# Performance work log

Measured on AMD Instinct MI355X. Metric: run time of the kernel, lower is better.

The kernel has to match this reference:

```python
import jax, jax.numpy as jnp
import numpy as np

N_NODES = 100000
N_EDGES = 1600000
D = 128


def setup_inputs() -> dict:
    key = jax.random.key(0)
    ks = jax.random.split(key, 6)
    x = jax.random.normal(ks[0], (N_NODES, D), dtype=jnp.float32)
    edge_index = jax.random.randint(ks[1], (2, N_EDGES), 0, N_NODES, dtype=jnp.int32)
    # nn.Linear weights: [out, in], bias [out]
    W1 = jax.random.normal(ks[2], (D, D), dtype=jnp.float32) * (1.0 / np.sqrt(D))
    b1 = jax.random.normal(ks[3], (D,), dtype=jnp.float32) * 0.01
    W2 = jax.random.normal(ks[4], (D, D), dtype=jnp.float32) * (1.0 / np.sqrt(D))
    b2 = jax.random.normal(ks[5], (D,), dtype=jnp.float32) * 0.01
    return {"x": x, "edge_index": edge_index, "W1": W1, "b1": b1, "W2": W2, "b2": b2}


def _gin_conv(x, src, dst, W, b, num_nodes):
    # sum aggregation of source features into destination nodes
    agg = jax.ops.segment_sum(x[src], dst, num_segments=num_nodes)  # [N, d]
    # eps = 0 (PyG GINConv default): (1+eps)*x_i + sum_j x_j, then Linear
    return (x + agg) @ W.T + b


def reference(x, edge_index, W1, b1, W2, b2):
    src, dst = edge_index[0], edge_index[1]
    n = x.shape[0]
    hid = _gin_conv(x, src, dst, W1, b1, n)
    out = _gin_conv(hid, src, dst, W2, b2, n)
    return (out, hid)
```

## Files before the change

kernel.cpp:

```cpp
#include <hip/hip_runtime.h>


#define DFEAT 128
#define BSHIFT 8
#define NB_MAX 512
#define CAP 8192
#define LROWS 136
#define AGG_BLOCKS 2048

typedef __attribute__((ext_vector_type(8))) short short8;
typedef __attribute__((ext_vector_type(4))) float f32x4;

__device__ __forceinline__ float bf2f(unsigned short u) {
    union { unsigned int i; float f; } c;
    c.i = ((unsigned int)u) << 16;
    return c.f;
}
__device__ __forceinline__ unsigned short f2b(float f) {
    union { float f; unsigned int i; } c;
    c.f = f;
    unsigned int u = c.i;
    u = (u + 0x7FFFu + ((u >> 16) & 1u)) >> 16;
    return (unsigned short)u;
}


__global__ __launch_bounds__(256) void scatter_cast(const int* __restrict__ src,
                                                    const int* __restrict__ dst,
                                                    int* __restrict__ bcur,
                                                    int* __restrict__ ebuf, int E,
                                                    int nscat,
                                                    const float* __restrict__ x,
                                                    unsigned short* __restrict__ xb,
                                                    int total4, int nzero) {
    int tid = threadIdx.x;
    if (blockIdx.x >= nscat) {
        int i = (blockIdx.x - nscat) * 256 + tid;
        if (i < total4) {
            float4 v = ((const float4*)x)[i];
            ushort4 o;
            o.x = f2b(v.x); o.y = f2b(v.y); o.z = f2b(v.z); o.w = f2b(v.w);
            ((ushort4*)xb)[i] = o;
        }
        if (blockIdx.x == nscat && tid < 32)
            ((ushort4*)xb)[(size_t)nzero * 32 + tid] = make_ushort4(0, 0, 0, 0);
        return;
    }
    __shared__ int lh[NB_MAX];
    for (int i = tid; i < NB_MAX; i += 256) lh[i] = 0;
    __syncthreads();
    int e0 = blockIdx.x * 4096;
    int e1 = min(e0 + 4096, E);
    int s[16], d[16];
    #pragma unroll
    for (int j = 0; j < 16; j++) {
        int e = e0 + tid + 256 * j;
        if (e < e1) { s[j] = src[e]; d[j] = dst[e]; atomicAdd(&lh[d[j] >> BSHIFT], 1); }
    }
    __syncthreads();
    for (int i = tid; i < NB_MAX; i += 256) {
        int c = lh[i];
        lh[i] = c ? (i * CAP + atomicAdd(&bcur[i], c)) : 0;
    }
    __syncthreads();
    #pragma unroll
    for (int j = 0; j < 16; j++) {
        int e = e0 + tid + 256 * j;
        if (e < e1) {
            int b = d[j] >> BSHIFT;
            int p = atomicAdd(&lh[b], 1);
            if (p < (b + 1) * CAP) ebuf[p] = (s[j] << 8) | (d[j] & 255);
        }
    }
}


__global__ __launch_bounds__(256) void csr_prep(const int* __restrict__ ebuf,
                                                const int* __restrict__ bcur,
                                                int2* __restrict__ rpse,
                                                int* __restrict__ esrc, int n, int nbk,
                                                const float* __restrict__ W1,
                                                const float* __restrict__ W2,
                                                const float* __restrict__ b1,
                                                unsigned short* __restrict__ Wb1,
                                                unsigned short* __restrict__ Wcb,
                                                float* __restrict__ w2b1) {
    int tid = threadIdx.x;
    if (blockIdx.x >= nbk) {
        __shared__ float red[256];
        int bb = blockIdx.x - nbk;
        int i = bb * 2 + (tid >> 7);
        int j = tid & 127;
        float s = 0.f;
        #pragma unroll 4
        for (int k = 0; k < 128; k++) s += W2[i * 128 + k] * W1[k * 128 + j];
        Wcb[i * 128 + j] = f2b(s);
        Wb1[i * 128 + j] = f2b(W1[i * 128 + j]);
        red[tid] = W2[i * 128 + j] * b1[j];
        __syncthreads();
        if (j == 0) {
            float t = 0.f;
            for (int k = 0; k < 128; k++) t += red[tid + k];
            w2b1[i] = t;
        }
        return;
    }
    __shared__ int hist[256];
    __shared__ int wsum[4];
    __shared__ int woff2[4];
    int b = blockIdx.x;
    int nbase = b << BSHIFT;
    int e0 = b * CAP;
    int e1 = e0 + min(bcur[b], CAP);
    hist[tid] = 0;
    __syncthreads();
    for (int e = e0 + tid; e < e1; e += 256)
        atomicAdd(&hist[ebuf[e] & 255], 1);
    __syncthreads();
    int v = hist[tid];
    int lane = tid & 63, wid = tid >> 6;
    int inc = v;
    #pragma unroll
    for (int off = 1; off < 64; off <<= 1) {
        int u = __shfl_up(inc, off, 64);
        if (lane >= off) inc += u;
    }
    if (lane == 63) wsum[wid] = inc;
    __syncthreads();
    if (tid == 0) {
        int run = 0;
        #pragma unroll
        for (int w = 0; w < 4; w++) { woff2[w] = run; run += wsum[w]; }
    }
    __syncthreads();
    int excl = woff2[wid] + inc - v;
    int node = nbase + tid;
    if (node < n) rpse[node] = make_int2(e0 + excl, e0 + excl + v);
    __syncthreads();
    hist[tid] = excl;
    __syncthreads();
    for (int e = e0 + tid; e < e1; e += 256) {
        int le = ebuf[e];
        int p = atomicAdd(&hist[le & 255], 1);
        esrc[e0 + p] = ((unsigned int)le) >> 8;
    }
}


__global__ __launch_bounds__(256) void fused_agg_gemm1(
        const ushort4* __restrict__ zin4, const int2* __restrict__ rpse,
        const int* __restrict__ esrc, const unsigned short* __restrict__ Wb,
        const float* __restrict__ bias, unsigned short* __restrict__ zout,
        float* __restrict__ out, int n, int ntiles) {
    __shared__ __align__(16) short lt[16 * LROWS];
    int w = threadIdx.x >> 6;
    int wl = threadIdx.x & 63;
    int gl = wl & 15, q = wl >> 4;
    int gbase = wl & 48;
    unsigned lb = (unsigned)gl * 16u;
    int lrow = w * 4 + q;
    const char* zb = (const char*)zin4;
    const int stride = gridDim.x;

    if (blockIdx.x == 0 && threadIdx.x < 16) {
        short8 z8;
        #pragma unroll
        for (int t = 0; t < 8; t++) z8[t] = 0;
        *(short8*)((char*)zout + (unsigned)n * 256u + threadIdx.x * 16) = z8;
    }

    float bb[2];
    #pragma unroll
    for (int cc = 0; cc < 2; cc++) bb[cc] = bias[(w * 2 + cc) * 16 + gl];

    int t = blockIdx.x;
    int node = t * 16 + lrow;
    int2 se = make_int2(0, 0);
    if (t < ntiles && node < n) se = rpse[node];
    int deg0 = se.y - se.x;
    int ei0 = (t < ntiles && node < n && gl < deg0) ? esrc[se.x + gl] : n;
    int ei1 = (t < ntiles && node < n && gl + 16 < deg0) ? esrc[se.x + gl + 16] : n;

    for (; t < ntiles; ) {
        int tn = t + stride;
        int node_n = tn * 16 + lrow;
        int2 se_n = make_int2(0, 0);
        if (tn < ntiles && node_n < n) se_n = rpse[node_n];

        int node_c = node < n ? node : n;
        float a[8];
        short8 sv = *(const short8*)(zb + (unsigned)node_c * 256u + lb);
        #pragma unroll
        for (int tt = 0; tt < 8; tt++) a[tt] = bf2f((unsigned short)sv[tt]);

        unsigned off[16];
        short8 vv[16];
        #pragma unroll
        for (int k = 0; k < 16; k++)
            off[k] = (unsigned)__shfl(ei0, gbase + k) * 256u + lb;
        #pragma unroll
        for (int k = 0; k < 16; k++) vv[k] = *(const short8*)(zb + off[k]);

        int deg_n = se_n.y - se_n.x;
        int ei0_n = n, ei1_n = n;
        if (tn < ntiles && node_n < n) {
            if (gl < deg_n)      ei0_n = esrc[se_n.x + gl];
            if (gl + 16 < deg_n) ei1_n = esrc[se_n.x + gl + 16];
        }

        #pragma unroll
        for (int k = 0; k < 16; k++) {
            #pragma unroll
            for (int tt = 0; tt < 8; tt++) a[tt] += bf2f((unsigned short)vv[k][tt]);
        }
        int deg = se.y - se.x;
        if (deg > 16) {
            unsigned o2[16];
            short8 v2[16];
            #pragma unroll
            for (int k = 0; k < 16; k++)
                o2[k] = (unsigned)__shfl(ei1, gbase + k) * 256u + lb;
            #pragma unroll
            for (int k = 0; k < 16; k++) v2[k] = *(const short8*)(zb + o2[k]);
            #pragma unroll
            for (int k = 0; k < 16; k++) {
                #pragma unroll
                for (int tt = 0; tt < 8; tt++) a[tt] += bf2f((unsigned short)v2[k][tt]);
            }
        }
        for (int rb = 32; rb < deg; rb += 16) {
            int eidx = (rb + gl < deg) ? esrc[se.x + rb + gl] : n;
            unsigned o2[16];
            short8 v2[16];
            #pragma unroll
            for (int k = 0; k < 16; k++)
                o2[k] = (unsigned)__shfl(eidx, gbase + k) * 256u + lb;
            #pragma unroll
            for (int k = 0; k < 16; k++) v2[k] = *(const short8*)(zb + o2[k]);
            #pragma unroll
            for (int k = 0; k < 16; k++) {
                #pragma unroll
                for (int tt = 0; tt < 8; tt++) a[tt] += bf2f((unsigned short)v2[k][tt]);
            }
        }

        short8 o;
        #pragma unroll
        for (int tt = 0; tt < 8; tt++) o[tt] = (short)f2b(a[tt]);
        *(short8*)((char*)lt + lrow * (LROWS * 2) + lb) = o;
        if (node < n) *(short8*)((char*)zout + (unsigned)node * 256u + lb) = o;
        __syncthreads();

        int m = gl;
        const short* ap = lt + m * LROWS + q * 8;
        short8 a0 = *(const short8*)(ap);
        short8 a1 = *(const short8*)(ap + 32);
        short8 a2 = *(const short8*)(ap + 64);
        short8 a3 = *(const short8*)(ap + 96);
        f32x4 acc[2];
        #pragma unroll
        for (int cc = 0; cc < 2; cc++) acc[cc] = (f32x4){0.f, 0.f, 0.f, 0.f};
        #pragma unroll
        for (int cc = 0; cc < 2; cc++) {
            int c = w * 2 + cc;
            const short* wp = (const short*)Wb + (c * 16 + m) * 128 + q * 8;
            short8 b0 = *(const short8*)(wp);
            short8 b1v = *(const short8*)(wp + 32);
            short8 b2v = *(const short8*)(wp + 64);
            short8 b3v = *(const short8*)(wp + 96);
            acc[cc] = __builtin_amdgcn_mfma_f32_16x16x32_bf16(a0, b0, acc[cc], 0, 0, 0);
            acc[cc] = __builtin_amdgcn_mfma_f32_16x16x32_bf16(a1, b1v, acc[cc], 0, 0, 0);
            acc[cc] = __builtin_amdgcn_mfma_f32_16x16x32_bf16(a2, b2v, acc[cc], 0, 0, 0);
            acc[cc] = __builtin_amdgcn_mfma_f32_16x16x32_bf16(a3, b3v, acc[cc], 0, 0, 0);
        }
        int row0 = t * 16 + q * 4;
        #pragma unroll
        for (int cc = 0; cc < 2; cc++) {
            int col = (w * 2 + cc) * 16 + m;
            #pragma unroll
            for (int r = 0; r < 4; r++) {
                int nd = row0 + r;
                if (nd < n) out[(size_t)nd * 128 + col] = acc[cc][r] + bb[cc];
            }
        }
        __syncthreads();

        se = se_n; ei0 = ei0_n; ei1 = ei1_n; node = node_n; t = tn;
    }
}

__global__ __launch_bounds__(256) void fused_agg_gemm2(
        const ushort4* __restrict__ zin4, const int2* __restrict__ rpse,
        const int* __restrict__ esrc, const unsigned short* __restrict__ Wb,
        const float* __restrict__ w2b1, const float* __restrict__ bias2,
        float* __restrict__ out, int n, int ntiles) {
    __shared__ __align__(16) short lt[16 * LROWS];
    int w = threadIdx.x >> 6;
    int wl = threadIdx.x & 63;
    int gl = wl & 15, q = wl >> 4;
    int gbase = wl & 48;
    unsigned lb = (unsigned)gl * 16u;
    int lrow = w * 4 + q;
    const char* zb = (const char*)zin4;
    const int stride = gridDim.x;

    float wb2[2], bb2[2];
    #pragma unroll
    for (int cc = 0; cc < 2; cc++) {
        int col = (w * 2 + cc) * 16 + gl;
        wb2[cc] = w2b1[col];
        bb2[cc] = bias2[col];
    }

    int t = blockIdx.x;
    int node = t * 16 + lrow;
    int2 se = make_int2(0, 0);
    if (t < ntiles && node < n) se = rpse[node];
    int deg0 = se.y - se.x;
    int ei0 = (t < ntiles && node < n && gl < deg0) ? esrc[se.x + gl] : n;
    int ei1 = (t < ntiles && node < n && gl + 16 < deg0) ? esrc[se.x + gl + 16] : n;

    for (; t < ntiles; ) {
        int tn = t + stride;
        int node_n = tn * 16 + lrow;
        int2 se_n = make_int2(0, 0);
        if (tn < ntiles && node_n < n) se_n = rpse[node_n];

        int node_c = node < n ? node : n;
        float a[8];
        short8 sv = *(const short8*)(zb + (unsigned)node_c * 256u + lb);
        #pragma unroll
        for (int tt = 0; tt < 8; tt++) a[tt] = bf2f((unsigned short)sv[tt]);

        unsigned off[16];
        short8 vv[16];
        #pragma unroll
        for (int k = 0; k < 16; k++)
            off[k] = (unsigned)__shfl(ei0, gbase + k) * 256u + lb;
        #pragma unroll
        for (int k = 0; k < 16; k++) vv[k] = *(const short8*)(zb + off[k]);

        int deg_n = se_n.y - se_n.x;
        int ei0_n = n, ei1_n = n;
        if (tn < ntiles && node_n < n) {
            if (gl < deg_n)      ei0_n = esrc[se_n.x + gl];
            if (gl + 16 < deg_n) ei1_n = esrc[se_n.x + gl + 16];
        }

        #pragma unroll
        for (int k = 0; k < 16; k++) {
            #pragma unroll
            for (int tt = 0; tt < 8; tt++) a[tt] += bf2f((unsigned short)vv[k][tt]);
        }
        int deg = se.y - se.x;
        if (deg > 16) {
            unsigned o2[16];
            short8 v2[16];
            #pragma unroll
            for (int k = 0; k < 16; k++)
                o2[k] = (unsigned)__shfl(ei1, gbase + k) * 256u + lb;
            #pragma unroll
            for (int k = 0; k < 16; k++) v2[k] = *(const short8*)(zb + o2[k]);
            #pragma unroll
            for (int k = 0; k < 16; k++) {
                #pragma unroll
                for (int tt = 0; tt < 8; tt++) a[tt] += bf2f((unsigned short)v2[k][tt]);
            }
        }
        for (int rb = 32; rb < deg; rb += 16) {
            int eidx = (rb + gl < deg) ? esrc[se.x + rb + gl] : n;
            unsigned o2[16];
            short8 v2[16];
            #pragma unroll
            for (int k = 0; k < 16; k++)
                o2[k] = (unsigned)__shfl(eidx, gbase + k) * 256u + lb;
            #pragma unroll
            for (int k = 0; k < 16; k++) v2[k] = *(const short8*)(zb + o2[k]);
            #pragma unroll
            for (int k = 0; k < 16; k++) {
                #pragma unroll
                for (int tt = 0; tt < 8; tt++) a[tt] += bf2f((unsigned short)v2[k][tt]);
            }
        }

        short8 o;
        #pragma unroll
        for (int tt = 0; tt < 8; tt++) o[tt] = (short)f2b(a[tt]);
        *(short8*)((char*)lt + lrow * (LROWS * 2) + lb) = o;
        __syncthreads();

        int m = gl;
        const short* ap = lt + m * LROWS + q * 8;
        short8 a0 = *(const short8*)(ap);
        short8 a1 = *(const short8*)(ap + 32);
        short8 a2 = *(const short8*)(ap + 64);
        short8 a3 = *(const short8*)(ap + 96);
        f32x4 acc[2];
        #pragma unroll
        for (int cc = 0; cc < 2; cc++) acc[cc] = (f32x4){0.f, 0.f, 0.f, 0.f};
        #pragma unroll
        for (int cc = 0; cc < 2; cc++) {
            int c = w * 2 + cc;
            const short* wp = (const short*)Wb + (c * 16 + m) * 128 + q * 8;
            short8 b0 = *(const short8*)(wp);
            short8 b1v = *(const short8*)(wp + 32);
            short8 b2v = *(const short8*)(wp + 64);
            short8 b3v = *(const short8*)(wp + 96);
            acc[cc] = __builtin_amdgcn_mfma_f32_16x16x32_bf16(a0, b0, acc[cc], 0, 0, 0);
            acc[cc] = __builtin_amdgcn_mfma_f32_16x16x32_bf16(a1, b1v, acc[cc], 0, 0, 0);
            acc[cc] = __builtin_amdgcn_mfma_f32_16x16x32_bf16(a2, b2v, acc[cc], 0, 0, 0);
            acc[cc] = __builtin_amdgcn_mfma_f32_16x16x32_bf16(a3, b3v, acc[cc], 0, 0, 0);
        }
        int row0 = t * 16 + q * 4;
        float degf[4];
        #pragma unroll
        for (int r = 0; r < 4; r++) {
            int nd = row0 + r;
            if (nd < n) {
                int2 s2 = rpse[nd];
                degf[r] = (float)(1 + s2.y - s2.x);
            } else degf[r] = 0.f;
        }
        #pragma unroll
        for (int cc = 0; cc < 2; cc++) {
            int col = (w * 2 + cc) * 16 + m;
            #pragma unroll
            for (int r = 0; r < 4; r++) {
                int nd = row0 + r;
                if (nd < n) out[(size_t)nd * 128 + col] = acc[cc][r] + degf[r] * wb2[cc] + bb2[cc];
            }
        }
        __syncthreads();

        se = se_n; ei0 = ei0_n; ei1 = ei1_n; node = node_n; t = tn;
    }
}


extern "C" void kernel_launch(void* const* d_in, const int* in_sizes, int n_in,
                              void* d_out, int out_size, void* d_ws, size_t ws_size,
                              hipStream_t stream) {
    const float* x  = (const float*)d_in[0];
    const int*   ei = (const int*)d_in[1];
    const float* W1 = (const float*)d_in[2];
    const float* b1 = (const float*)d_in[3];
    const float* W2 = (const float*)d_in[4];
    const float* b2 = (const float*)d_in[5];

    const int n = in_sizes[0] / DFEAT;
    const int E = in_sizes[1] / 2;
    const int* src = ei;
    const int* dst = ei + E;
    const int nbuckets = (n + (1 << BSHIFT) - 1) >> BSHIFT;

    float* out = (float*)d_out;
    float* hid = out + (size_t)n * DFEAT;

    unsigned short* xb = (unsigned short*)out;

    char* w = (char*)d_ws;
    const size_t szB = (size_t)n * DFEAT * sizeof(unsigned short);
    const size_t szB1 = szB + 4096;
    unsigned short* z1b = (unsigned short*)w;
    int* ebuf = (int*)(w + szB1);
    int* esrc = (int*)(w + szB1 + szB);
    int2* rpse = (int2*)(esrc + (size_t)nbuckets * CAP);
    int* bcur = (int*)(rpse + n);
    char* wp = (char*)(bcur + NB_MAX);
    unsigned short* Wb1 = (unsigned short*)wp;
    unsigned short* Wcb = Wb1 + DFEAT * DFEAT;
    float* w2b1 = (float*)(Wcb + DFEAT * DFEAT);

    const int cast_blocks = (n * 32 + 255) / 256;
    hipMemsetAsync(bcur, 0, nbuckets * sizeof(int), stream);
    scatter_cast<<<nbuckets + cast_blocks, 256, 0, stream>>>(
        src, dst, bcur, ebuf, E, nbuckets, x, xb, n * 32, n);
    csr_prep<<<nbuckets + 64, 256, 0, stream>>>(
        ebuf, bcur, rpse, esrc, n, nbuckets, W1, W2, b1, Wb1, Wcb, w2b1);

    const int ntiles = (n + 15) / 16;
    const int fb = AGG_BLOCKS;
    fused_agg_gemm1<<<fb, 256, 0, stream>>>(
        (const ushort4*)xb, rpse, esrc, Wb1, b1, z1b, hid, n, ntiles);
    fused_agg_gemm2<<<fb, 256, 0, stream>>>(
        (const ushort4*)z1b, rpse, esrc, Wcb, w2b1, b2, out, n, ntiles);
}
```

Baseline: 326.2 us.

## Fuse CSR bucket sort into first aggregation+GEMM kernel with 64-node buckets

Destination buckets shrink from 256 to 64 nodes. The per-bucket counting sort now runs inside the first aggregation/GEMM kernel, which keeps the sorted source list in shared memory and still writes rpse and esrc for the second layer. The weight preprocessing moves into the scatter/cast kernel, so one launch and a round trip of esrc through global memory are removed. The cost is a larger shared-memory footprint per block and no cross-tile prefetch of edge indices. Per-bucket capacity also drops to 2048 edges, which leaves less headroom for skewed degree distributions.

```diff
diff --git a/kernel.cpp b/kernel.cpp
--- a/kernel.cpp
+++ b/kernel.cpp
@@ -2,9 +2,10 @@
 
 
 #define DFEAT 128
-#define BSHIFT 8
-#define NB_MAX 512
-#define CAP 8192
+#define BSHIFT 6
+#define BNODES 64
+#define NB_MAX 2048
+#define CAP 2048
 #define LROWS 136
 #define AGG_BLOCKS 2048
 
@@ -25,70 +26,30 @@
 }
 
 
-__global__ __launch_bounds__(256) void scatter_cast(const int* __restrict__ src,
-                                                    const int* __restrict__ dst,
-                                                    int* __restrict__ bcur,
-                                                    int* __restrict__ ebuf, int E,
-                                                    int nscat,
-                                                    const float* __restrict__ x,
-                                                    unsigned short* __restrict__ xb,
-                                                    int total4, int nzero) {
+__global__ __launch_bounds__(256) void scatter_cast_prep(
+        const int* __restrict__ src, const int* __restrict__ dst,
+        int* __restrict__ bcur, int* __restrict__ ebuf, int E, int nscat, int nbk,
+        const float* __restrict__ x, unsigned short* __restrict__ xb,
+        int total4, int nzero,
+        const float* __restrict__ W1, const float* __restrict__ W2,
+        const float* __restrict__ b1, unsigned short* __restrict__ Wb1,
+        unsigned short* __restrict__ Wcb, float* __restrict__ w2b1) {
     int tid = threadIdx.x;
-    if (blockIdx.x >= nscat) {
-        int i = (blockIdx.x - nscat) * 256 + tid;
+    if (blockIdx.x >= nscat + 64) {
+        int i = (blockIdx.x - nscat - 64) * 256 + tid;
         if (i < total4) {
             float4 v = ((const float4*)x)[i];
             ushort4 o;
             o.x = f2b(v.x); o.y = f2b(v.y); o.z = f2b(v.z); o.w = f2b(v.w);
             ((ushort4*)xb)[i] = o;
         }
-        if (blockIdx.x == nscat && tid < 32)
+        if (blockIdx.x == nscat + 64 && tid < 32)
             ((ushort4*)xb)[(size_t)nzero * 32 + tid] = make_ushort4(0, 0, 0, 0);
         return;
     }
-    __shared__ int lh[NB_MAX];
-    for (int i = tid; i < NB_MAX; i += 256) lh[i] = 0;
-    __syncthreads();
-    int e0 = blockIdx.x * 4096;
-    int e1 = min(e0 + 4096, E);
-    int s[16], d[16];
-    #pragma unroll
-    for (int j = 0; j < 16; j++) {
-        int e = e0 + tid + 256 * j;
-        if (e < e1) { s[j] = src[e]; d[j] = dst[e]; atomicAdd(&lh[d[j] >> BSHIFT], 1); }
-    }
-    __syncthreads();
-    for (int i = tid; i < NB_MAX; i += 256) {
-        int c = lh[i];
-        lh[i] = c ? (i * CAP + atomicAdd(&bcur[i], c)) : 0;
-    }
-    __syncthreads();
-    #pragma unroll
-    for (int j = 0; j < 16; j++) {
-        int e = e0 + tid + 256 * j;
-        if (e < e1) {
-            int b = d[j] >> BSHIFT;
-            int p = atomicAdd(&lh[b], 1);
-            if (p < (b + 1) * CAP) ebuf[p] = (s[j] << 8) | (d[j] & 255);
-        }
-    }
-}
-
-
-__global__ __launch_bounds__(256) void csr_prep(const int* __restrict__ ebuf,
-                                                const int* __restrict__ bcur,
-                                                int2* __restrict__ rpse,
-                                                int* __restrict__ esrc, int n, int nbk,
-                                                const float* __restrict__ W1,
-                                                const float* __restrict__ W2,
-                                                const float* __restrict__ b1,
-                                                unsigned short* __restrict__ Wb1,
-                                                unsigned short* __restrict__ Wcb,
-                                                float* __restrict__ w2b1) {
-    int tid = threadIdx.x;
-    if (blockIdx.x >= nbk) {
+    if (blockIdx.x >= nscat) {
         __shared__ float red[256];
-        int bb = blockIdx.x - nbk;
+        int bb = blockIdx.x - nscat;
         int i = bb * 2 + (tid >> 7);
         int j = tid & 127;
         float s = 0.f;
@@ -105,154 +66,172 @@
         }
         return;
     }
-    __shared__ int hist[256];
-    __shared__ int wsum[4];
-    __shared__ int woff2[4];
+    __shared__ int lh[NB_MAX];
+    for (int i = tid; i < nbk; i += 256) lh[i] = 0;
+    __syncthreads();
+    int e0 = blockIdx.x * 4096;
+    int e1 = min(e0 + 4096, E);
+    int s[16], d[16];
+    #pragma unroll
+    for (int j = 0; j < 16; j++) {
+        int e = e0 + tid + 256 * j;
+        if (e < e1) { s[j] = src[e]; d[j] = dst[e]; atomicAdd(&lh[d[j] >> BSHIFT], 1); }
+    }
+    __syncthreads();
+    for (int i = tid; i < nbk; i += 256) {
+        int c = lh[i];
+        lh[i] = c ? (i * CAP + atomicAdd(&bcur[i], c)) : 0;
+    }
+    __syncthreads();
+    #pragma unroll
+    for (int j = 0; j < 16; j++) {
+        int e = e0 + tid + 256 * j;
+        if (e < e1) {
+            int b = d[j] >> BSHIFT;
+            int p = atomicAdd(&lh[b], 1);
+            if (p < (b + 1) * CAP) ebuf[p] = (s[j] << 6) | (d[j] & 63);
+        }
+    }
+}
+
+
+__global__ __launch_bounds__(256) void fused_csr_agg_gemm1(
+        const int* __restrict__ ebuf, const int* __restrict__ bcur,
+        const ushort4* __restrict__ zin4, const unsigned short* __restrict__ Wb,
+        const float* __restrict__ bias, int2* __restrict__ rpse,
+        int* __restrict__ esrc, unsigned short* __restrict__ zout,
+        float* __restrict__ out, int n) {
+    __shared__ int esrc_s[CAP];
+    __shared__ __align__(16) short lt[64 * LROWS];
+    __shared__ int cursor[64];
+    __shared__ int exl_s[64];
+    __shared__ int deg_s[64];
+    int tid = threadIdx.x;
     int b = blockIdx.x;
-    int nbase = b << BSHIFT;
-    int e0 = b * CAP;
-    int e1 = e0 + min(bcur[b], CAP);
-    hist[tid] = 0;
-    __syncthreads();
-    for (int e = e0 + tid; e < e1; e += 256)
-        atomicAdd(&hist[ebuf[e] & 255], 1);
-    __syncthreads();
-    int v = hist[tid];
-    int lane = tid & 63, wid = tid >> 6;
-    int inc = v;
-    #pragma unroll
-    for (int off = 1; off < 64; off <<= 1) {
-        int u = __shfl_up(inc, off, 64);
-        if (lane >= off) inc += u;
-    }
-    if (lane == 63) wsum[wid] = inc;
-    __syncthreads();
-    if (tid == 0) {
-        int run = 0;
-        #pragma unroll
-        for (int w = 0; w < 4; w++) { woff2[w] = run; run += wsum[w]; }
-    }
-    __syncthreads();
-    int excl = woff2[wid] + inc - v;
-    int node = nbase + tid;
-    if (node < n) rpse[node] = make_int2(e0 + excl, e0 + excl + v);
-    __syncthreads();
-    hist[tid] = excl;
-    __syncthreads();
-    for (int e = e0 + tid; e < e1; e += 256) {
-        int le = ebuf[e];
-        int p = atomicAdd(&hist[le & 255], 1);
-        esrc[e0 + p] = ((unsigned int)le) >> 8;
-    }
-}
-
-
-__global__ __launch_bounds__(256) void fused_agg_gemm1(
-        const ushort4* __restrict__ zin4, const int2* __restrict__ rpse,
-        const int* __restrict__ esrc, const unsigned short* __restrict__ Wb,
-        const float* __restrict__ bias, unsigned short* __restrict__ zout,
-        float* __restrict__ out, int n, int ntiles) {
-    __shared__ __align__(16) short lt[16 * LROWS];
-    int w = threadIdx.x >> 6;
-    int wl = threadIdx.x & 63;
+    int e0b = b * CAP;
+    int cnt = min(bcur[b], CAP);
+
+    if (b == 0 && tid < 16) {
+        short8 z8;
+        #pragma unroll
+        for (int t = 0; t < 8; t++) z8[t] = 0;
+        *(short8*)((char*)zout + (unsigned)n * 256u + tid * 16) = z8;
+    }
+
+    if (tid < 64) cursor[tid] = 0;
+    __syncthreads();
+    for (int e = tid; e < cnt; e += 256)
+        atomicAdd(&cursor[ebuf[e0b + e] & 63], 1);
+    __syncthreads();
+    if (tid < 64) {
+        int v = cursor[tid];
+        int inc = v;
+        #pragma unroll
+        for (int off = 1; off < 64; off <<= 1) {
+            int u = __shfl_up(inc, off, 64);
+            if (tid >= off) inc += u;
+        }
+        int excl = inc - v;
+        exl_s[tid] = excl;
+        deg_s[tid] = v;
+        int node = b * 64 + tid;
+        if (node < n) rpse[node] = make_int2(e0b + excl, e0b + excl + v);
+    }
+    __syncthreads();
+    if (tid < 64) cursor[tid] = exl_s[tid];
+    __syncthreads();
+    for (int e = tid; e < cnt; e += 256) {
+        int le = ebuf[e0b + e];
+        int p = atomicAdd(&cursor[le & 63], 1);
+        int sv = ((unsigned)le) >> 6;
+        esrc_s[p] = sv;
+        esrc[e0b + p] = sv;
+    }
+    __syncthreads();
+
+    int w = tid >> 6, wl = tid & 63;
     int gl = wl & 15, q = wl >> 4;
     int gbase = wl & 48;
     unsigned lb = (unsigned)gl * 16u;
-    int lrow = w * 4 + q;
     const char* zb = (const char*)zin4;
-    const int stride = gridDim.x;
-
-    if (blockIdx.x == 0 && threadIdx.x < 16) {
-        short8 z8;
-        #pragma unroll
-        for (int t = 0; t < 8; t++) z8[t] = 0;
-        *(short8*)((char*)zout + (unsigned)n * 256u + threadIdx.x * 16) = z8;
-    }
-
+    for (int it = 0; it < 4; ++it) {
+        int li = w * 16 + it * 4 + q;
+        int node = b * 64 + li;
+        int deg = deg_s[li], eb = exl_s[li];
+        int node_c = node < n ? node : n;
+        float a[8];
+        short8 svr = *(const short8*)(zb + (unsigned)node_c * 256u + lb);
+        #pragma unroll
+        for (int tt = 0; tt < 8; tt++) a[tt] = bf2f((unsigned short)svr[tt]);
+        int ei0 = (gl < deg) ? esrc_s[eb + gl] : n;
+        int ei1 = (gl + 16 < deg) ? esrc_s[eb + gl + 16] : n;
+        {
+            unsigned off[16];
+            short8 vv[16];
+            #pragma unroll
+            for (int k = 0; k < 16; k++)
+                off[k] = (unsigned)__shfl(ei0, gbase + k) * 256u + lb;
+            #pragma unroll
+            for (int k = 0; k < 16; k++) vv[k] = *(const short8*)(zb + off[k]);
+            #pragma unroll
+            for (int k = 0; k < 16; k++) {
+                #pragma unroll
+                for (int tt = 0; tt < 8; tt++) a[tt] += bf2f((unsigned short)vv[k][tt]);
+            }
+        }
+        if (deg > 16) {
+            unsigned off[16];
+            short8 vv[16];
+            #pragma unroll
+            for (int k = 0; k < 16; k++)
+                off[k] = (unsigned)__shfl(ei1, gbase + k) * 256u + lb;
+            #pragma unroll
+            for (int k = 0; k < 16; k++) vv[k] = *(const short8*)(zb + off[k]);
+            #pragma unroll
+            for (int k = 0; k < 16; k++) {
+                #pragma unroll
+                for (int tt = 0; tt < 8; tt++) a[tt] += bf2f((unsigned short)vv[k][tt]);
+            }
+        }
+        for (int rb = 32; rb < deg; rb += 16) {
+            int eidx = (rb + gl < deg) ? esrc_s[eb + rb + gl] : n;
+            unsigned off[16];
+            short8 vv[16];
+            #pragma unroll
+            for (int k = 0; k < 16; k++)
+                off[k] = (unsigned)__shfl(eidx, gbase + k) * 256u + lb;
+            #pragma unroll
+            for (int k = 0; k < 16; k++) vv[k] = *(const short8*)(zb + off[k]);
+            #pragma unroll
+            for (int k = 0; k < 16; k++) {
+                #pragma unroll
+                for (int tt = 0; tt < 8; tt++) a[tt] += bf2f((unsigned short)vv[k][tt]);
+            }
+        }
+        short8 o;
+        #pragma unroll
+        for (int tt = 0; tt < 8; tt++) o[tt] = (short)f2b(a[tt]);
+        *(short8*)((char*)lt + li * (LROWS * 2) + lb) = o;
+        if (node < n) *(short8*)((char*)zout + (unsigned)node * 256u + lb) = o;
+    }
+    __syncthreads();
+
+    int m = gl;
+    short8 B[2][4];
     float bb[2];
     #pragma unroll
-    for (int cc = 0; cc < 2; cc++) bb[cc] = bias[(w * 2 + cc) * 16 + gl];
-
-    int t = blockIdx.x;
-    int node = t * 16 + lrow;
-    int2 se = make_int2(0, 0);
-    if (t < ntiles && node < n) se = rpse[node];
-    int deg0 = se.y - se.x;
-    int ei0 = (t < ntiles && node < n && gl < deg0) ? esrc[se.x + gl] : n;
-    int ei1 = (t < ntiles && node < n && gl + 16 < deg0) ? esrc[se.x + gl + 16] : n;
-
-    for (; t < ntiles; ) {
-        int tn = t + stride;
-        int node_n = tn * 16 + lrow;
-        int2 se_n = make_int2(0, 0);
-        if (tn < ntiles && node_n < n) se_n = rpse[node_n];
-
-        int node_c = node < n ? node : n;
-        float a[8];
-        short8 sv = *(const short8*)(zb + (unsigned)node_c * 256u + lb);
-        #pragma unroll
-        for (int tt = 0; tt < 8; tt++) a[tt] = bf2f((unsigned short)sv[tt]);
-
-        unsigned off[16];
-        short8 vv[16];
-        #pragma unroll
-        for (int k = 0; k < 16; k++)
-            off[k] = (unsigned)__shfl(ei0, gbase + k) * 256u + lb;
-        #pragma unroll
-        for (int k = 0; k < 16; k++) vv[k] = *(const short8*)(zb + off[k]);
-
-        int deg_n = se_n.y - se_n.x;
-        int ei0_n = n, ei1_n = n;
-        if (tn < ntiles && node_n < n) {
-            if (gl < deg_n)      ei0_n = esrc[se_n.x + gl];
-            if (gl + 16 < deg_n) ei1_n = esrc[se_n.x + gl + 16];
-        }
-
-        #pragma unroll
-        for (int k = 0; k < 16; k++) {
-            #pragma unroll
-            for (int tt = 0; tt < 8; tt++) a[tt] += bf2f((unsigned short)vv[k][tt]);
-        }
-        int deg = se.y - se.x;
-        if (deg > 16) {
-            unsigned o2[16];
-            short8 v2[16];
-            #pragma unroll
-            for (int k = 0; k < 16; k++)
-                o2[k] = (unsigned)__shfl(ei1, gbase + k) * 256u + lb;
-            #pragma unroll
-            for (int k = 0; k < 16; k++) v2[k] = *(const short8*)(zb + o2[k]);
-            #pragma unroll
-            for (int k = 0; k < 16; k++) {
-                #pragma unroll
-                for (int tt = 0; tt < 8; tt++) a[tt] += bf2f((unsigned short)v2[k][tt]);
-            }
-        }
-        for (int rb = 32; rb < deg; rb += 16) {
-            int eidx = (rb + gl < deg) ? esrc[se.x + rb + gl] : n;
-            unsigned o2[16];
-            short8 v2[16];
-            #pragma unroll
-            for (int k = 0; k < 16; k++)
-                o2[k] = (unsigned)__shfl(eidx, gbase + k) * 256u + lb;
-            #pragma unroll
-            for (int k = 0; k < 16; k++) v2[k] = *(const short8*)(zb + o2[k]);
-            #pragma unroll
-            for (int k = 0; k < 16; k++) {
-                #pragma unroll
-                for (int tt = 0; tt < 8; tt++) a[tt] += bf2f((unsigned short)v2[k][tt]);
-            }
-        }
-
-        short8 o;
-        #pragma unroll
-        for (int tt = 0; tt < 8; tt++) o[tt] = (short)f2b(a[tt]);
-        *(short8*)((char*)lt + lrow * (LROWS * 2) + lb) = o;
-        if (node < n) *(short8*)((char*)zout + (unsigned)node * 256u + lb) = o;
-        __syncthreads();
-
-        int m = gl;
-        const short* ap = lt + m * LROWS + q * 8;
+    for (int cc = 0; cc < 2; cc++) {
+        int c = w * 2 + cc;
+        const short* wp = (const short*)Wb + (c * 16 + m) * 128 + q * 8;
+        B[cc][0] = *(const short8*)(wp);
+        B[cc][1] = *(const short8*)(wp + 32);
+        B[cc][2] = *(const short8*)(wp + 64);
+        B[cc][3] = *(const short8*)(wp + 96);
+        bb[cc] = bias[c * 16 + m];
+    }
+    #pragma unroll
+    for (int st = 0; st < 4; ++st) {
+        const short* ap = lt + (st * 16 + m) * LROWS + q * 8;
         short8 a0 = *(const short8*)(ap);
         short8 a1 = *(const short8*)(ap + 32);
         short8 a2 = *(const short8*)(ap + 64);
@@ -262,18 +241,12 @@
         for (int cc = 0; cc < 2; cc++) acc[cc] = (f32x4){0.f, 0.f, 0.f, 0.f};
         #pragma unroll
         for (int cc = 0; cc < 2; cc++) {
-            int c = w * 2 + cc;
-            const short* wp = (const short*)Wb + (c * 16 + m) * 128 + q * 8;
-            short8 b0 = *(const short8*)(wp);
-            short8 b1v = *(const short8*)(wp + 32);
-            short8 b2v = *(const short8*)(wp + 64);
-            short8 b3v = *(const short8*)(wp + 96);
-            acc[cc] = __builtin_amdgcn_mfma_f32_16x16x32_bf16(a0, b0, acc[cc], 0, 0, 0);
-            acc[cc] = __builtin_amdgcn_mfma_f32_16x16x32_bf16(a1, b1v, acc[cc], 0, 0, 0);
-            acc[cc] = __builtin_amdgcn_mfma_f32_16x16x32_bf16(a2, b2v, acc[cc], 0, 0, 0);
-            acc[cc] = __builtin_amdgcn_mfma_f32_16x16x32_bf16(a3, b3v, acc[cc], 0, 0, 0);
-        }
-        int row0 = t * 16 + q * 4;
+            acc[cc] = __builtin_amdgcn_mfma_f32_16x16x32_bf16(a0, B[cc][0], acc[cc], 0, 0, 0);
+            acc[cc] = __builtin_amdgcn_mfma_f32_16x16x32_bf16(a1, B[cc][1], acc[cc], 0, 0, 0);
+            acc[cc] = __builtin_amdgcn_mfma_f32_16x16x32_bf16(a2, B[cc][2], acc[cc], 0, 0, 0);
+            acc[cc] = __builtin_amdgcn_mfma_f32_16x16x32_bf16(a3, B[cc][3], acc[cc], 0, 0, 0);
+        }
+        int row0 = b * 64 + st * 16 + q * 4;
         #pragma unroll
         for (int cc = 0; cc < 2; cc++) {
             int col = (w * 2 + cc) * 16 + m;
@@ -283,11 +256,9 @@
                 if (nd < n) out[(size_t)nd * 128 + col] = acc[cc][r] + bb[cc];
             }
         }
-        __syncthreads();
-
-        se = se_n; ei0 = ei0_n; ei1 = ei1_n; node = node_n; t = tn;
-    }
-}
+    }
+}
+
 
 __global__ __launch_bounds__(256) void fused_agg_gemm2(
         const ushort4* __restrict__ zin4, const int2* __restrict__ rpse,
@@ -451,7 +422,7 @@
     const int E = in_sizes[1] / 2;
     const int* src = ei;
     const int* dst = ei + E;
-    const int nbuckets = (n + (1 << BSHIFT) - 1) >> BSHIFT;
+    const int nbuckets = (n + BNODES - 1) / BNODES;
 
     float* out = (float*)d_out;
     float* hid = out + (size_t)n * DFEAT;
@@ -471,17 +442,17 @@
     unsigned short* Wcb = Wb1 + DFEAT * DFEAT;
     float* w2b1 = (float*)(Wcb + DFEAT * DFEAT);
 
+    const int nscat = (E + 4095) / 4096;
     const int cast_blocks = (n * 32 + 255) / 256;
     hipMemsetAsync(bcur, 0, nbuckets * sizeof(int), stream);
-    scatter_cast<<<nbuckets + cast_blocks, 256, 0, stream>>>(
-        src, dst, bcur, ebuf, E, nbuckets, x, xb, n * 32, n);
-    csr_prep<<<nbuckets + 64, 256, 0, stream>>>(
-        ebuf, bcur, rpse, esrc, n, nbuckets, W1, W2, b1, Wb1, Wcb, w2b1);
+    scatter_cast_prep<<<nscat + 64 + cast_blocks, 256, 0, stream>>>(
+        src, dst, bcur, ebuf, E, nscat, nbuckets, x, xb, n * 32, n,
+        W1, W2, b1, Wb1, Wcb, w2b1);
+
+    fused_csr_agg_gemm1<<<nbuckets, 256, 0, stream>>>(
+        ebuf, bcur, (const ushort4*)xb, Wb1, b1, rpse, esrc, z1b, hid, n);
 
     const int ntiles = (n + 15) / 16;
-    const int fb = AGG_BLOCKS;
-    fused_agg_gemm1<<<fb, 256, 0, stream>>>(
-        (const ushort4*)xb, rpse, esrc, Wb1, b1, z1b, hid, n, ntiles);
-    fused_agg_gemm2<<<fb, 256, 0, stream>>>(
+    fused_agg_gemm2<<<AGG_BLOCKS, 256, 0, stream>>>(
         (const ushort4*)z1b, rpse, esrc, Wcb, w2b1, b2, out, n, ntiles);
 }
```

Measured after the change: 328.3 us. Within noise of the previous version (+0.6%).

## Split CSR prep per bucket into four quarter-blocks for more parallelism

Applied to the files above, without the earlier changes.

The CSR build kernel now launches four blocks per destination bucket. Each block handles the 64 destination nodes of one quarter and writes into a fixed QCAP-sized sub-region of the bucket's edge range. This raises block count and parallelism in the histogram, scan and scatter phases. The cost is that each block rereads the whole bucket's edge buffer, so those reads happen four times. A quarter holding more than QCAP edges would spill into the next quarter's region. The scatter kernel's grid size is now derived from the edge count instead of the bucket count.

```diff
diff --git a/kernel.cpp b/kernel.cpp
--- a/kernel.cpp
+++ b/kernel.cpp
@@ -5,6 +5,7 @@
 #define BSHIFT 8
 #define NB_MAX 512
 #define CAP 8192
+#define QCAP 2048
 #define LROWS 136
 #define AGG_BLOCKS 2048
 
@@ -75,20 +76,20 @@
 }
 
 
-__global__ __launch_bounds__(256) void csr_prep(const int* __restrict__ ebuf,
-                                                const int* __restrict__ bcur,
-                                                int2* __restrict__ rpse,
-                                                int* __restrict__ esrc, int n, int nbk,
-                                                const float* __restrict__ W1,
-                                                const float* __restrict__ W2,
-                                                const float* __restrict__ b1,
-                                                unsigned short* __restrict__ Wb1,
-                                                unsigned short* __restrict__ Wcb,
-                                                float* __restrict__ w2b1) {
+__global__ __launch_bounds__(256) void csr_prep_q(const int* __restrict__ ebuf,
+                                                  const int* __restrict__ bcur,
+                                                  int2* __restrict__ rpse,
+                                                  int* __restrict__ esrc, int n, int nq,
+                                                  const float* __restrict__ W1,
+                                                  const float* __restrict__ W2,
+                                                  const float* __restrict__ b1,
+                                                  unsigned short* __restrict__ Wb1,
+                                                  unsigned short* __restrict__ Wcb,
+                                                  float* __restrict__ w2b1) {
     int tid = threadIdx.x;
-    if (blockIdx.x >= nbk) {
+    if (blockIdx.x >= nq) {
         __shared__ float red[256];
-        int bb = blockIdx.x - nbk;
+        int bb = blockIdx.x - nq;
         int i = bb * 2 + (tid >> 7);
         int j = tid & 127;
         float s = 0.f;
@@ -105,44 +106,42 @@
         }
         return;
     }
-    __shared__ int hist[256];
-    __shared__ int wsum[4];
-    __shared__ int woff2[4];
-    int b = blockIdx.x;
-    int nbase = b << BSHIFT;
-    int e0 = b * CAP;
-    int e1 = e0 + min(bcur[b], CAP);
-    hist[tid] = 0;
-    __syncthreads();
-    for (int e = e0 + tid; e < e1; e += 256)
-        atomicAdd(&hist[ebuf[e] & 255], 1);
-    __syncthreads();
-    int v = hist[tid];
-    int lane = tid & 63, wid = tid >> 6;
-    int inc = v;
-    #pragma unroll
-    for (int off = 1; off < 64; off <<= 1) {
-        int u = __shfl_up(inc, off, 64);
-        if (lane >= off) inc += u;
-    }
-    if (lane == 63) wsum[wid] = inc;
-    __syncthreads();
-    if (tid == 0) {
-        int run = 0;
-        #pragma unroll
-        for (int w = 0; w < 4; w++) { woff2[w] = run; run += wsum[w]; }
-    }
-    __syncthreads();
-    int excl = woff2[wid] + inc - v;
-    int node = nbase + tid;
-    if (node < n) rpse[node] = make_int2(e0 + excl, e0 + excl + v);
-    __syncthreads();
-    hist[tid] = excl;
-    __syncthreads();
-    for (int e = e0 + tid; e < e1; e += 256) {
-        int le = ebuf[e];
-        int p = atomicAdd(&hist[le & 255], 1);
-        esrc[e0 + p] = ((unsigned int)le) >> 8;
+    __shared__ int hist[64];
+    __shared__ int excl_s[64];
+    int b = blockIdx.x, cb = b >> 2, qq = b & 3;
+    int e0 = cb * CAP;
+    int cnt = min(bcur[cb], CAP);
+    int qbase = e0 + qq * QCAP;
+    if (tid < 64) hist[tid] = 0;
+    __syncthreads();
+    for (int e = tid; e < cnt; e += 256) {
+        int d = ebuf[e0 + e] & 255;
+        if ((d >> 6) == qq) atomicAdd(&hist[d & 63], 1);
+    }
+    __syncthreads();
+    if (tid < 64) {
+        int v = hist[tid];
+        int inc = v;
+        #pragma unroll
+        for (int off = 1; off < 64; off <<= 1) {
+            int u = __shfl_up(inc, off, 64);
+            if (tid >= off) inc += u;
+        }
+        int excl = inc - v;
+        excl_s[tid] = excl;
+        int node = cb * 256 + qq * 64 + tid;
+        if (node < n) rpse[node] = make_int2(qbase + excl, qbase + excl + v);
+    }
+    __syncthreads();
+    if (tid < 64) hist[tid] = excl_s[tid];
+    __syncthreads();
+    for (int e = tid; e < cnt; e += 256) {
+        int code = ebuf[e0 + e];
+        int d = code & 255;
+        if ((d >> 6) == qq) {
+            int p = atomicAdd(&hist[d & 63], 1);
+            esrc[qbase + p] = ((unsigned)code) >> 8;
+        }
     }
 }
 
@@ -451,7 +450,7 @@
     const int E = in_sizes[1] / 2;
     const int* src = ei;
     const int* dst = ei + E;
-    const int nbuckets = (n + (1 << BSHIFT) - 1) >> BSHIFT;
+    const int nbuckets = (n + 255) >> BSHIFT;
 
     float* out = (float*)d_out;
     float* hid = out + (size_t)n * DFEAT;
@@ -471,17 +470,19 @@
     unsigned short* Wcb = Wb1 + DFEAT * DFEAT;
     float* w2b1 = (float*)(Wcb + DFEAT * DFEAT);
 
+    const int nscat = (E + 4095) / 4096;
     const int cast_blocks = (n * 32 + 255) / 256;
     hipMemsetAsync(bcur, 0, nbuckets * sizeof(int), stream);
-    scatter_cast<<<nbuckets + cast_blocks, 256, 0, stream>>>(
-        src, dst, bcur, ebuf, E, nbuckets, x, xb, n * 32, n);
-    csr_prep<<<nbuckets + 64, 256, 0, stream>>>(
-        ebuf, bcur, rpse, esrc, n, nbuckets, W1, W2, b1, Wb1, Wcb, w2b1);
+    scatter_cast<<<nscat + cast_blocks, 256, 0, stream>>>(
+        src, dst, bcur, ebuf, E, nscat, x, xb, n * 32, n);
+
+    const int nq = nbuckets * 4;
+    csr_prep_q<<<nq + 64, 256, 0, stream>>>(
+        ebuf, bcur, rpse, esrc, n, nq, W1, W2, b1, Wb1, Wcb, w2b1);
 
     const int ntiles = (n + 15) / 16;
-    const int fb = AGG_BLOCKS;
-    fused_agg_gemm1<<<fb, 256, 0, stream>>>(
+    fused_agg_gemm1<<<AGG_BLOCKS, 256, 0, stream>>>(
         (const ushort4*)xb, rpse, esrc, Wb1, b1, z1b, hid, n, ntiles);
-    fused_agg_gemm2<<<fb, 256, 0, stream>>>(
+    fused_agg_gemm2<<<AGG_BLOCKS, 256, 0, stream>>>(
         (const ushort4*)z1b, rpse, esrc, Wcb, w2b1, b2, out, n, ntiles);
 }
```

Result: no change. 327.1 us (+0.3%).
